# Optimization experiments

Hardware: AMD Instinct MI355X
Metric: run time of the kernel (lower is better)

Reference implementation:

```python
import jax, jax.numpy as jnp
import numpy as np

C = 128
K = 7
RED = 4
C_RED = C // RED
PAD = (K - 1) // 2
BN_EPS = 1e-5


def setup_inputs() -> dict:
    key = jax.random.key(0)
    ks = jax.random.split(key, 7)
    b, h, w = 8, 56, 56
    x = jax.random.normal(ks[0], (b, C, h, w), dtype=jnp.float32)
    # 1x1 conv #1: c -> c_red
    w1 = jax.random.normal(ks[1], (C_RED, C), dtype=jnp.float32) * (1.0 / np.sqrt(C))
    b1 = jax.random.normal(ks[2], (C_RED,), dtype=jnp.float32) * 0.01
    # BatchNorm affine params
    gamma = jnp.ones((C_RED,), dtype=jnp.float32)
    beta = jnp.zeros((C_RED,), dtype=jnp.float32)
    # 1x1 conv #2: c_red -> k*k
    w2 = jax.random.normal(ks[3], (K * K, C_RED), dtype=jnp.float32) * (1.0 / np.sqrt(C_RED))
    b2 = jax.random.normal(ks[4], (K * K,), dtype=jnp.float32) * 0.01
    return {"x": x, "w1": w1, "b1": b1, "gamma": gamma, "beta": beta, "w2": w2, "b2": b2}


def _unfold(x):
    # torch.nn.Unfold(K, padding=PAD, stride=1) -> (b, c, k*k, h, w), channel-major
    b, c, h, w = x.shape
    xp = jnp.pad(x, ((0, 0), (0, 0), (PAD, PAD), (PAD, PAD)))
    patches = [xp[:, :, i:i + h, j:j + w] for i in range(K) for j in range(K)]
    return jnp.stack(patches, axis=2)  # (b, c, k*k, h, w)


def reference(x, w1, b1, gamma, beta, w2, b2):
    b, c, h, w = x.shape
    # kernel-generation branch: 1x1 conv -> BN (batch stats, training mode) -> ReLU -> 1x1 conv
    t = jnp.einsum('rc,bchw->brhw', w1, x) + b1[None, :, None, None]
    mean = t.mean(axis=(0, 2, 3))
    var = t.var(axis=(0, 2, 3))  # biased, as in torch BN normalization
    t = (t - mean[None, :, None, None]) * jax.lax.rsqrt(var + BN_EPS)[None, :, None, None]
    t = jax.nn.relu(t * gamma[None, :, None, None] + beta[None, :, None, None])
    kern = jnp.einsum('kr,brhw->bkhw', w2, t) + b2[None, :, None, None]  # (b, k*k, h, w)
    # involution: per-pixel kernel broadcast over channels, sum over k*k taps
    x_unf = _unfold(x)  # (b, c, k*k, h, w)
    return jnp.einsum('bkhw,bckhw->bchw', kern, x_unf)
```

## Files before the change

### kernel.cpp

```cpp
#include <hip/hip_runtime.h>

#define C 128
#define CRED 32
#define K 7
#define KK 49
#define H 56
#define W 56
#define P (H*W)
#define B 8
#define NPIX (B*P)
#define BN_EPS 1e-5

#define T_OFF 0
#define T_SIZE (B*CRED*P)
#define KERN_OFF (T_OFF + T_SIZE)
#define KERN_SIZE (B*KK*P)
#define NBLK_A (49*B)
#define PSUM_OFF (KERN_OFF + KERN_SIZE)
#define PSQ_OFF (PSUM_OFF + NBLK_A*CRED)
#define SS_OFF  (PSQ_OFF + NBLK_A*CRED)
#define SCALE_OFF SS_OFF
#define SHIFT_OFF (SS_OFF + CRED)
#define WS_NEED ((size_t)(SHIFT_OFF + CRED) * sizeof(float))

#define FB_SCALE_OFF T_SIZE
#define FB_SHIFT_OFF (T_SIZE + CRED)

__global__ __launch_bounds__(256) void kA_conv1(const float* __restrict__ x,
                                                const float* __restrict__ w1,
                                                const float* __restrict__ b1,
                                                float* __restrict__ ws) {
    int tid = threadIdx.x;
    int bx = blockIdx.x;
    int b  = blockIdx.y;
    int px = tid & 63;
    int p  = bx * 64 + px;
    int ru8 = __builtin_amdgcn_readfirstlane((tid >> 6) * 8);
    const float* __restrict__ wq = w1 + (size_t)ru8 * C;
    const float* xb = x + (size_t)b * C * P + p;

    float acc[8];
#pragma unroll
    for (int u = 0; u < 8; ++u) acc[u] = 0.f;
#pragma unroll 8
    for (int c = 0; c < C; ++c) {
        float xv = xb[(size_t)c * P];
#pragma unroll
        for (int u = 0; u < 8; ++u)
            acc[u] = fmaf(wq[u * C + c], xv, acc[u]);
    }
#pragma unroll
    for (int u = 0; u < 8; ++u) acc[u] += b1[ru8 + u];

    float* tb = ws + T_OFF + (size_t)b * CRED * P + p;
#pragma unroll
    for (int u = 0; u < 8; ++u)
        tb[(size_t)(ru8 + u) * P] = acc[u];

    float s[8], q[8];
#pragma unroll
    for (int u = 0; u < 8; ++u) { s[u] = acc[u]; q[u] = acc[u] * acc[u]; }
#pragma unroll
    for (int off = 32; off; off >>= 1) {
#pragma unroll
        for (int u = 0; u < 8; ++u) {
            s[u] += __shfl_xor(s[u], off);
            q[u] += __shfl_xor(q[u], off);
        }
    }
    if (px == 0) {
        int blk = b * 49 + bx;
        float* psum = ws + PSUM_OFF + (size_t)blk * CRED + ru8;
        float* psq  = ws + PSQ_OFF  + (size_t)blk * CRED + ru8;
#pragma unroll
        for (int u = 0; u < 8; ++u) { psum[u] = s[u]; psq[u] = q[u]; }
    }
}

__global__ __launch_bounds__(256) void kB_bnfin(const float* __restrict__ gamma,
                                                const float* __restrict__ beta,
                                                float* __restrict__ ws) {
    __shared__ double sd1[8][CRED];
    __shared__ double sd2[8][CRED];
    int tid = threadIdx.x;
    int r = tid & 31, g = tid >> 5;
    double s1 = 0.0, s2 = 0.0;
    for (int i = g * 49; i < g * 49 + 49; ++i) {
        s1 += (double)ws[PSUM_OFF + i * CRED + r];
        s2 += (double)ws[PSQ_OFF + i * CRED + r];
    }
    sd1[g][r] = s1; sd2[g][r] = s2;
    __syncthreads();
    if (tid < CRED) {
        double S1 = 0.0, S2 = 0.0;
        for (int gg = 0; gg < 8; ++gg) { S1 += sd1[gg][tid]; S2 += sd2[gg][tid]; }
        double mean = S1 / NPIX;
        double var = S2 / NPIX - mean * mean;
        double sc = (double)gamma[tid] / sqrt(var + BN_EPS);
        ws[SCALE_OFF + tid] = (float)sc;
        ws[SHIFT_OFF + tid] = (float)((double)beta[tid] - mean * sc);
    }
}

__global__ __launch_bounds__(256) void kC_kern(const float* __restrict__ w2,
                                               const float* __restrict__ b2,
                                               float* __restrict__ ws) {
    __shared__ float s_t[CRED * W];
    __shared__ float s_w2[KK * 33];
    int tid = threadIdx.x;
    int h = blockIdx.x, b = blockIdx.y;
    for (int i = tid; i < KK * CRED; i += 256) {
        int k = i >> 5, r = i & 31;
        s_w2[k * 33 + r] = w2[i];
    }
    const float* scale = ws + SCALE_OFF;
    const float* shift = ws + SHIFT_OFF;
    for (int i = tid; i < CRED * W; i += 256) {
        int r = i / W, w = i - r * W;
        float v = ws[T_OFF + ((size_t)b * CRED + r) * P + h * W + w];
        v = fmaf(v, scale[r], shift[r]);
        s_t[r * W + w] = fmaxf(v, 0.f);
    }
    __syncthreads();
    for (int i = tid; i < KK * 14; i += 256) {
        int k = i / 14, w0 = (i - k * 14) * 4;
        float bb = b2[k];
        float a0 = bb, a1 = bb, a2 = bb, a3 = bb;
#pragma unroll
        for (int r = 0; r < CRED; ++r) {
            float4 tv = *(const float4*)&s_t[r * W + w0];
            float wv = s_w2[k * 33 + r];
            a0 = fmaf(wv, tv.x, a0);
            a1 = fmaf(wv, tv.y, a1);
            a2 = fmaf(wv, tv.z, a2);
            a3 = fmaf(wv, tv.w, a3);
        }
        float4 o = {a0, a1, a2, a3};
        *(float4*)&ws[KERN_OFF + ((size_t)b * KK + k) * P + h * W + w0] = o;
    }
}

#define TH 8
#define XROWS 14
#define XPITCH 68
__global__ __launch_bounds__(448) void kD_inv(const float* __restrict__ x,
                                              const float* __restrict__ ws,
                                              float* __restrict__ out) {
    __shared__ float4 s_x[2][XROWS * XPITCH];
    int tid = threadIdx.x;
    int bx = blockIdx.x;
    int z  = blockIdx.y;
    int b = bx / 7, ht = bx - b * 7;
    int h0 = ht * TH;
    int orow = tid / W;
    int ocol = tid - orow * W;
    int sbase = orow * XPITCH + ocol;

    float kr[KK];
    {
        const float* kb = ws + KERN_OFF + (size_t)b * KK * P + (size_t)h0 * W + tid;
#pragma unroll
        for (int k = 0; k < KK; ++k) kr[k] = kb[(size_t)k * P];
    }

    int slot0, slot1, off0, off1, v0, v1;
    {
        int q = tid;
        int row = q >> 6, col = q & 63;
        int hh = h0 - 3 + row, ww = col - 3;
        v0 = ((unsigned)hh < H && (unsigned)ww < W);
        off0 = hh * W + ww;
        slot0 = row * XPITCH + col;
        q = tid + 448;
        row = q >> 6; col = q & 63;
        hh = h0 - 3 + row; ww = col - 3;
        v1 = ((unsigned)hh < H && (unsigned)ww < W);
        off1 = hh * W + ww;
        slot1 = row * XPITCH + col;
    }

    int cg0 = z * 16;
    const size_t xbase = ((size_t)b * C + cg0) * P;
    {
        const float* xc = x + xbase;
        float4 f0, f1;
        f0.x = v0 ? xc[off0] : 0.f;  f0.y = v0 ? xc[P + off0] : 0.f;
        f0.z = v0 ? xc[2 * P + off0] : 0.f;  f0.w = v0 ? xc[3 * P + off0] : 0.f;
        f1.x = v1 ? xc[off1] : 0.f;  f1.y = v1 ? xc[P + off1] : 0.f;
        f1.z = v1 ? xc[2 * P + off1] : 0.f;  f1.w = v1 ? xc[3 * P + off1] : 0.f;
        s_x[0][slot0] = f0;
        s_x[0][slot1] = f1;
    }

    for (int it = 0; it < 4; ++it) {
        __syncthreads();
        float4 n0, n1;
        if (it < 3) {
            const float* xc = x + xbase + (size_t)(it + 1) * 4 * P;
            n0.x = v0 ? xc[off0] : 0.f;  n0.y = v0 ? xc[P + off0] : 0.f;
            n0.z = v0 ? xc[2 * P + off0] : 0.f;  n0.w = v0 ? xc[3 * P + off0] : 0.f;
            n1.x = v1 ? xc[off1] : 0.f;  n1.y = v1 ? xc[P + off1] : 0.f;
            n1.z = v1 ? xc[2 * P + off1] : 0.f;  n1.w = v1 ? xc[3 * P + off1] : 0.f;
        }
        const float4* xs = s_x[it & 1] + sbase;
        float a0 = 0.f, a1 = 0.f, a2 = 0.f, a3 = 0.f;
#pragma unroll
        for (int i = 0; i < K; ++i) {
#pragma unroll
            for (int j = 0; j < K; ++j) {
                float4 xv = xs[i * XPITCH + j];
                float kv = kr[i * 7 + j];
                a0 = fmaf(kv, xv.x, a0);
                a1 = fmaf(kv, xv.y, a1);
                a2 = fmaf(kv, xv.z, a2);
                a3 = fmaf(kv, xv.w, a3);
            }
        }
        float* ob = out + xbase + (size_t)it * 4 * P + (size_t)h0 * W + tid;
        ob[0]     = a0;
        ob[P]     = a1;
        ob[2 * P] = a2;
        ob[3 * P] = a3;
        if (it < 3) {
            float4* nb = s_x[(it + 1) & 1];
            nb[slot0] = n0;
            nb[slot1] = n1;
        }
    }
}

__global__ __launch_bounds__(256) void k1_conv1(const float* __restrict__ x,
                                                const float* __restrict__ w1,
                                                const float* __restrict__ b1,
                                                float* __restrict__ t) {
    __shared__ float s_w1t[C * CRED];
    int tid = threadIdx.x;
    for (int i = tid; i < C * CRED; i += 256) {
        int c = i >> 5, r = i & 31;
        s_w1t[i] = w1[r * C + c];
    }
    __syncthreads();
    int b = blockIdx.y;
    int p = blockIdx.x * 256 + tid;
    if (p >= P) return;
    float acc[CRED];
#pragma unroll
    for (int r = 0; r < CRED; ++r) acc[r] = 0.f;
    const float* xb = x + (size_t)b * C * P + p;
    for (int c = 0; c < C; ++c) {
        float xv = xb[(size_t)c * P];
#pragma unroll
        for (int r = 0; r < CRED; ++r)
            acc[r] = fmaf(s_w1t[c * CRED + r], xv, acc[r]);
    }
    float* tb = t + (size_t)b * CRED * P + p;
#pragma unroll
    for (int r = 0; r < CRED; ++r)
        tb[(size_t)r * P] = acc[r] + b1[r];
}

__global__ __launch_bounds__(256) void k2_bnstats(const float* __restrict__ t,
                                                  const float* __restrict__ gamma,
                                                  const float* __restrict__ beta,
                                                  float* __restrict__ scale,
                                                  float* __restrict__ shift) {
    int r = blockIdx.x;
    int tid = threadIdx.x;
    double s = 0.0, s2 = 0.0;
    for (int i = tid; i < NPIX; i += 256) {
        int b = i / P, p = i - b * P;
        float v = t[((size_t)b * CRED + r) * P + p];
        s += v;
        s2 += (double)v * v;
    }
    __shared__ double ls[256], ls2[256];
    ls[tid] = s; ls2[tid] = s2;
    __syncthreads();
    for (int off = 128; off > 0; off >>= 1) {
        if (tid < off) { ls[tid] += ls[tid + off]; ls2[tid] += ls2[tid + off]; }
        __syncthreads();
    }
    if (tid == 0) {
        double mean = ls[0] / NPIX;
        double var = ls2[0] / NPIX - mean * mean;
        double sc = (double)gamma[r] / sqrt(var + BN_EPS);
        scale[r] = (float)sc;
        shift[r] = (float)((double)beta[r] - mean * sc);
    }
}

__global__ __launch_bounds__(256) void k3_involution(const float* __restrict__ x,
                                                     const float* __restrict__ t,
                                                     const float* __restrict__ scale,
                                                     const float* __restrict__ shift,
                                                     const float* __restrict__ w2,
                                                     const float* __restrict__ b2,
                                                     float* __restrict__ out) {
    int h = blockIdx.x;
    int b = blockIdx.y;
    int z = blockIdx.z;
    int tid = threadIdx.x;
    __shared__ float s_w2[KK * CRED];
    __shared__ float s_t[CRED * W];
    __shared__ float s_kern[KK][W];
    __shared__ float s_x[4][K][64];
    for (int i = tid; i < KK * CRED; i += 256) s_w2[i] = w2[i];
    for (int i = tid; i < CRED * W; i += 256) {
        int r = i / W, w = i - r * W;
        float v = t[((size_t)b * CRED + r) * P + h * W + w];
        v = fmaf(v, scale[r], shift[r]);
        s_t[r * W + w] = fmaxf(v, 0.f);
    }
    __syncthreads();
    for (int i = tid; i < KK * W; i += 256) {
        int k = i / W, w = i - k * W;
        float acc = b2[k];
#pragma unroll
        for (int r = 0; r < CRED; ++r)
            acc = fmaf(s_w2[k * CRED + r], s_t[r * W + w], acc);
        s_kern[k][w] = acc;
    }
    __syncthreads();
    int w = tid % W;
    int c4 = tid / W;
    float kr[KK];
#pragma unroll
    for (int k = 0; k < KK; ++k) kr[k] = s_kern[k][w];
    int cbase = z * (C / 2);
    for (int cg = cbase; cg < cbase + C / 2; cg += 4) {
        for (int i = tid; i < 4 * K * 64; i += 256) {
            int col = i & 63;
            int rc = i >> 6;
            int cc = rc / K;
            int row = rc - cc * K;
            int hh = h - 3 + row;
            int ww = col - 3;
            float v = 0.f;
            if ((unsigned)hh < H && (unsigned)ww < W)
                v = x[(((size_t)b * C + cg + cc) * H + hh) * W + ww];
            s_x[cc][row][col] = v;
        }
        __syncthreads();
        if (tid < 4 * W) {
            float acc = 0.f;
#pragma unroll
            for (int i = 0; i < K; ++i)
#pragma unroll
                for (int j = 0; j < K; ++j)
                    acc = fmaf(kr[i * K + j], s_x[c4][i][w + j], acc);
            out[(((size_t)b * C + cg + c4) * H + h) * W + w] = acc;
        }
        __syncthreads();
    }
}

extern "C" void kernel_launch(void* const* d_in, const int* in_sizes, int n_in,
                              void* d_out, int out_size, void* d_ws, size_t ws_size,
                              hipStream_t stream) {
    const float* x     = (const float*)d_in[0];
    const float* w1    = (const float*)d_in[1];
    const float* b1    = (const float*)d_in[2];
    const float* gamma = (const float*)d_in[3];
    const float* beta  = (const float*)d_in[4];
    const float* w2    = (const float*)d_in[5];
    const float* b2    = (const float*)d_in[6];
    float* out = (float*)d_out;
    float* ws  = (float*)d_ws;

    if (ws_size >= WS_NEED) {
        dim3 gA(49, B);
        kA_conv1<<<gA, 256, 0, stream>>>(x, w1, b1, ws);
        kB_bnfin<<<1, 256, 0, stream>>>(gamma, beta, ws);
        dim3 gC(H, B);
        kC_kern<<<gC, 256, 0, stream>>>(w2, b2, ws);
        dim3 gD(7 * B, 8);
        kD_inv<<<gD, 448, 0, stream>>>(x, ws, out);
    } else {
        float* t     = ws;
        float* scale = ws + FB_SCALE_OFF;
        float* shift = ws + FB_SHIFT_OFF;
        dim3 g1((P + 255) / 256, B);
        k1_conv1<<<g1, 256, 0, stream>>>(x, w1, b1, t);
        k2_bnstats<<<CRED, 256, 0, stream>>>(t, gamma, beta, scale, shift);
        dim3 g3(H, B, 2);
        k3_involution<<<g3, 256, 0, stream>>>(x, t, scale, shift, w2, b2, out);
    }
}
```

Before: 44.42 us.

## Fuse BN finalize into kernel-gen kernel and retile involution to 7-row tiles

Removes the single-block BN finalize launch: every kernel-generation block now redundantly reduces the per-block partial sums to get scale and shift in shared memory, while loading the raw t tile in parallel. The involution kernel changes from 8-row to 7-row tiles (64 blocks per channel group), so 392 of 448 threads compute and the rest only help load the halo. Masked loads are replaced by clamped-offset loads multiplied by a 0/1 mask. This saves one launch and its serialization, at the cost of 448 blocks each repeating the 392x32 partial reduction in double precision and more involution blocks with idle threads.

```diff
diff --git a/kernel.cpp b/kernel.cpp
--- a/kernel.cpp
+++ b/kernel.cpp
@@ -77,49 +77,51 @@
     }
 }
 
-__global__ __launch_bounds__(256) void kB_bnfin(const float* __restrict__ gamma,
+__global__ __launch_bounds__(256) void kCB_kern(const float* __restrict__ w2,
+                                                const float* __restrict__ b2,
+                                                const float* __restrict__ gamma,
                                                 const float* __restrict__ beta,
                                                 float* __restrict__ ws) {
+    __shared__ float s_t[CRED * W];
+    __shared__ float s_w2[KK * 33];
     __shared__ double sd1[8][CRED];
     __shared__ double sd2[8][CRED];
-    int tid = threadIdx.x;
-    int r = tid & 31, g = tid >> 5;
-    double s1 = 0.0, s2 = 0.0;
-    for (int i = g * 49; i < g * 49 + 49; ++i) {
-        s1 += (double)ws[PSUM_OFF + i * CRED + r];
-        s2 += (double)ws[PSQ_OFF + i * CRED + r];
-    }
-    sd1[g][r] = s1; sd2[g][r] = s2;
+    __shared__ float s_sc[CRED];
+    __shared__ float s_sh[CRED];
+    int tid = threadIdx.x;
+    int h = blockIdx.x, b = blockIdx.y;
+
+    {
+        int r = tid & 31, seg = tid >> 5;
+        double s1 = 0.0, s2 = 0.0;
+        for (int i = seg * 49; i < seg * 49 + 49; ++i) {
+            s1 += (double)ws[PSUM_OFF + i * CRED + r];
+            s2 += (double)ws[PSQ_OFF + i * CRED + r];
+        }
+        sd1[seg][r] = s1; sd2[seg][r] = s2;
+    }
+    for (int i = tid; i < KK * CRED; i += 256) {
+        int k = i >> 5, r = i & 31;
+        s_w2[k * 33 + r] = w2[i];
+    }
+    for (int i = tid; i < CRED * W; i += 256) {
+        int r = i / W, w = i - r * W;
+        s_t[i] = ws[T_OFF + ((size_t)b * CRED + r) * P + h * W + w];
+    }
     __syncthreads();
     if (tid < CRED) {
         double S1 = 0.0, S2 = 0.0;
-        for (int gg = 0; gg < 8; ++gg) { S1 += sd1[gg][tid]; S2 += sd2[gg][tid]; }
+        for (int g = 0; g < 8; ++g) { S1 += sd1[g][tid]; S2 += sd2[g][tid]; }
         double mean = S1 / NPIX;
         double var = S2 / NPIX - mean * mean;
         double sc = (double)gamma[tid] / sqrt(var + BN_EPS);
-        ws[SCALE_OFF + tid] = (float)sc;
-        ws[SHIFT_OFF + tid] = (float)((double)beta[tid] - mean * sc);
-    }
-}
-
-__global__ __launch_bounds__(256) void kC_kern(const float* __restrict__ w2,
-                                               const float* __restrict__ b2,
-                                               float* __restrict__ ws) {
-    __shared__ float s_t[CRED * W];
-    __shared__ float s_w2[KK * 33];
-    int tid = threadIdx.x;
-    int h = blockIdx.x, b = blockIdx.y;
-    for (int i = tid; i < KK * CRED; i += 256) {
-        int k = i >> 5, r = i & 31;
-        s_w2[k * 33 + r] = w2[i];
-    }
-    const float* scale = ws + SCALE_OFF;
-    const float* shift = ws + SHIFT_OFF;
+        s_sc[tid] = (float)sc;
+        s_sh[tid] = (float)((double)beta[tid] - mean * sc);
+    }
+    __syncthreads();
     for (int i = tid; i < CRED * W; i += 256) {
-        int r = i / W, w = i - r * W;
-        float v = ws[T_OFF + ((size_t)b * CRED + r) * P + h * W + w];
-        v = fmaf(v, scale[r], shift[r]);
-        s_t[r * W + w] = fmaxf(v, 0.f);
+        int r = i / W;
+        s_t[i] = fmaxf(fmaf(s_t[i], s_sc[r], s_sh[r]), 0.f);
     }
     __syncthreads();
     for (int i = tid; i < KK * 14; i += 256) {
@@ -140,8 +142,8 @@
     }
 }
 
-#define TH 8
-#define XROWS 14
+#define TH 7
+#define XROWS 13
 #define XPITCH 68
 __global__ __launch_bounds__(448) void kD_inv(const float* __restrict__ x,
                                               const float* __restrict__ ws,
@@ -150,81 +152,83 @@
     int tid = threadIdx.x;
     int bx = blockIdx.x;
     int z  = blockIdx.y;
-    int b = bx / 7, ht = bx - b * 7;
+    int b = bx >> 3, ht = bx & 7;
     int h0 = ht * TH;
     int orow = tid / W;
     int ocol = tid - orow * W;
     int sbase = orow * XPITCH + ocol;
+    bool owns = orow < TH;
+
+    int q0 = tid, q1 = tid + 448;
+    int row0 = q0 >> 6, col0 = q0 & 63;
+    int hh0 = h0 - 3 + row0, ww0 = col0 - 3;
+    float m0 = ((unsigned)hh0 < H && (unsigned)ww0 < W) ? 1.f : 0.f;
+    int off0 = (m0 != 0.f) ? (hh0 * W + ww0) : 0;
+    int slot0 = row0 * XPITCH + col0;
+    int row1 = q1 >> 6, col1 = q1 & 63;
+    int hh1 = h0 - 3 + row1, ww1 = col1 - 3;
+    bool in1 = q1 < XROWS * 64;
+    float m1 = (in1 && (unsigned)hh1 < H && (unsigned)ww1 < W) ? 1.f : 0.f;
+    int off1 = (m1 != 0.f) ? (hh1 * W + ww1) : 0;
+    int slot1 = row1 * XPITCH + col1;
+
+    int cg0 = z * 16;
+    const size_t xbase = ((size_t)b * C + cg0) * P;
+
+    const float* xc0 = x + xbase;
+    float4 f0, f1;
+    f0.x = xc0[off0] * m0;          f0.y = xc0[P + off0] * m0;
+    f0.z = xc0[2 * P + off0] * m0;  f0.w = xc0[3 * P + off0] * m0;
+    f1.x = xc0[off1] * m1;          f1.y = xc0[P + off1] * m1;
+    f1.z = xc0[2 * P + off1] * m1;  f1.w = xc0[3 * P + off1] * m1;
 
     float kr[KK];
     {
-        const float* kb = ws + KERN_OFF + (size_t)b * KK * P + (size_t)h0 * W + tid;
+        int kidx = h0 * W + tid;
+        if (kidx > P - 1) kidx = P - 1;
+        const float* kb = ws + KERN_OFF + (size_t)b * KK * P + kidx;
 #pragma unroll
         for (int k = 0; k < KK; ++k) kr[k] = kb[(size_t)k * P];
     }
 
-    int slot0, slot1, off0, off1, v0, v1;
-    {
-        int q = tid;
-        int row = q >> 6, col = q & 63;
-        int hh = h0 - 3 + row, ww = col - 3;
-        v0 = ((unsigned)hh < H && (unsigned)ww < W);
-        off0 = hh * W + ww;
-        slot0 = row * XPITCH + col;
-        q = tid + 448;
-        row = q >> 6; col = q & 63;
-        hh = h0 - 3 + row; ww = col - 3;
-        v1 = ((unsigned)hh < H && (unsigned)ww < W);
-        off1 = hh * W + ww;
-        slot1 = row * XPITCH + col;
-    }
-
-    int cg0 = z * 16;
-    const size_t xbase = ((size_t)b * C + cg0) * P;
-    {
-        const float* xc = x + xbase;
-        float4 f0, f1;
-        f0.x = v0 ? xc[off0] : 0.f;  f0.y = v0 ? xc[P + off0] : 0.f;
-        f0.z = v0 ? xc[2 * P + off0] : 0.f;  f0.w = v0 ? xc[3 * P + off0] : 0.f;
-        f1.x = v1 ? xc[off1] : 0.f;  f1.y = v1 ? xc[P + off1] : 0.f;
-        f1.z = v1 ? xc[2 * P + off1] : 0.f;  f1.w = v1 ? xc[3 * P + off1] : 0.f;
-        s_x[0][slot0] = f0;
-        s_x[0][slot1] = f1;
-    }
+    s_x[0][slot0] = f0;
+    if (in1) s_x[0][slot1] = f1;
 
     for (int it = 0; it < 4; ++it) {
         __syncthreads();
         float4 n0, n1;
         if (it < 3) {
             const float* xc = x + xbase + (size_t)(it + 1) * 4 * P;
-            n0.x = v0 ? xc[off0] : 0.f;  n0.y = v0 ? xc[P + off0] : 0.f;
-            n0.z = v0 ? xc[2 * P + off0] : 0.f;  n0.w = v0 ? xc[3 * P + off0] : 0.f;
-            n1.x = v1 ? xc[off1] : 0.f;  n1.y = v1 ? xc[P + off1] : 0.f;
-            n1.z = v1 ? xc[2 * P + off1] : 0.f;  n1.w = v1 ? xc[3 * P + off1] : 0.f;
-        }
-        const float4* xs = s_x[it & 1] + sbase;
-        float a0 = 0.f, a1 = 0.f, a2 = 0.f, a3 = 0.f;
-#pragma unroll
-        for (int i = 0; i < K; ++i) {
-#pragma unroll
-            for (int j = 0; j < K; ++j) {
-                float4 xv = xs[i * XPITCH + j];
-                float kv = kr[i * 7 + j];
-                a0 = fmaf(kv, xv.x, a0);
-                a1 = fmaf(kv, xv.y, a1);
-                a2 = fmaf(kv, xv.z, a2);
-                a3 = fmaf(kv, xv.w, a3);
+            n0.x = xc[off0] * m0;          n0.y = xc[P + off0] * m0;
+            n0.z = xc[2 * P + off0] * m0;  n0.w = xc[3 * P + off0] * m0;
+            n1.x = xc[off1] * m1;          n1.y = xc[P + off1] * m1;
+            n1.z = xc[2 * P + off1] * m1;  n1.w = xc[3 * P + off1] * m1;
+        }
+        if (owns) {
+            const float4* xs = s_x[it & 1] + sbase;
+            float a0 = 0.f, a1 = 0.f, a2 = 0.f, a3 = 0.f;
+#pragma unroll
+            for (int i = 0; i < K; ++i) {
+#pragma unroll
+                for (int j = 0; j < K; ++j) {
+                    float4 xv = xs[i * XPITCH + j];
+                    float kv = kr[i * 7 + j];
+                    a0 = fmaf(kv, xv.x, a0);
+                    a1 = fmaf(kv, xv.y, a1);
+                    a2 = fmaf(kv, xv.z, a2);
+                    a3 = fmaf(kv, xv.w, a3);
+                }
             }
-        }
-        float* ob = out + xbase + (size_t)it * 4 * P + (size_t)h0 * W + tid;
-        ob[0]     = a0;
-        ob[P]     = a1;
-        ob[2 * P] = a2;
-        ob[3 * P] = a3;
+            float* ob = out + xbase + (size_t)it * 4 * P + (size_t)h0 * W + tid;
+            ob[0]     = a0;
+            ob[P]     = a1;
+            ob[2 * P] = a2;
+            ob[3 * P] = a3;
+        }
         if (it < 3) {
             float4* nb = s_x[(it + 1) & 1];
             nb[slot0] = n0;
-            nb[slot1] = n1;
+            if (in1) nb[slot1] = n1;
         }
     }
 }
@@ -370,10 +374,9 @@
     if (ws_size >= WS_NEED) {
         dim3 gA(49, B);
         kA_conv1<<<gA, 256, 0, stream>>>(x, w1, b1, ws);
-        kB_bnfin<<<1, 256, 0, stream>>>(gamma, beta, ws);
         dim3 gC(H, B);
-        kC_kern<<<gC, 256, 0, stream>>>(w2, b2, ws);
-        dim3 gD(7 * B, 8);
+        kCB_kern<<<gC, 256, 0, stream>>>(w2, b2, gamma, beta, ws);
+        dim3 gD(64, 8);
         kD_inv<<<gD, 448, 0, stream>>>(x, ws, out);
     } else {
         float* t     = ws;
```

New measurement: 48.46 us. 9.1% more time.

## Process 32 channels per block with single-shot LDS load in involution kernel

Applied to the files above, without the earlier changes.

The involution kernel now stages all 32 channels of a block's input tile into shared memory at once, instead of double-buffering 4 channels at a time over 16 channels. Each thread keeps 8 float4 accumulators and streams the per-pixel kernel weights from global memory per tap, so each weight read is reused across 32 channels. The grid is halved along the channel dimension. This removes the per-iteration barriers and reuses each weight more, but needs about 119 KB of LDS per block, which limits occupancy to one block per CU. The smaller grid also no longer covers all CUs, and the staging load no longer overlaps with compute.

```diff
diff --git a/kernel.cpp b/kernel.cpp
--- a/kernel.cpp
+++ b/kernel.cpp
@@ -143,10 +143,10 @@
 #define TH 8
 #define XROWS 14
 #define XPITCH 68
-__global__ __launch_bounds__(448) void kD_inv(const float* __restrict__ x,
-                                              const float* __restrict__ ws,
-                                              float* __restrict__ out) {
-    __shared__ float4 s_x[2][XROWS * XPITCH];
+__global__ __launch_bounds__(448) void kD2_inv(const float* __restrict__ x,
+                                               const float* __restrict__ ws,
+                                               float* __restrict__ out) {
+    __shared__ float4 s_x[XROWS * 8 * XPITCH];
     int tid = threadIdx.x;
     int bx = blockIdx.x;
     int z  = blockIdx.y;
@@ -154,78 +154,64 @@
     int h0 = ht * TH;
     int orow = tid / W;
     int ocol = tid - orow * W;
-    int sbase = orow * XPITCH + ocol;
-
-    float kr[KK];
-    {
-        const float* kb = ws + KERN_OFF + (size_t)b * KK * P + (size_t)h0 * W + tid;
-#pragma unroll
-        for (int k = 0; k < KK; ++k) kr[k] = kb[(size_t)k * P];
-    }
-
-    int slot0, slot1, off0, off1, v0, v1;
-    {
-        int q = tid;
-        int row = q >> 6, col = q & 63;
-        int hh = h0 - 3 + row, ww = col - 3;
-        v0 = ((unsigned)hh < H && (unsigned)ww < W);
-        off0 = hh * W + ww;
-        slot0 = row * XPITCH + col;
-        q = tid + 448;
-        row = q >> 6; col = q & 63;
-        hh = h0 - 3 + row; ww = col - 3;
-        v1 = ((unsigned)hh < H && (unsigned)ww < W);
-        off1 = hh * W + ww;
-        slot1 = row * XPITCH + col;
-    }
-
-    int cg0 = z * 16;
+
+    int row0 = tid >> 6, col0 = tid & 63;
+    int hh0 = h0 - 3 + row0, ww0 = col0 - 3;
+    float m0 = ((unsigned)hh0 < H && (unsigned)ww0 < W) ? 1.f : 0.f;
+    int off0 = (m0 != 0.f) ? (hh0 * W + ww0) : 0;
+    int hh1 = hh0 + 7;
+    float m1 = ((unsigned)hh1 < H && (unsigned)ww0 < W) ? 1.f : 0.f;
+    int off1 = (m1 != 0.f) ? (hh1 * W + ww0) : 0;
+    int slot0b = (row0 * 8) * XPITCH + col0;
+    int slot1b = ((row0 + 7) * 8) * XPITCH + col0;
+
+    int cg0 = z * 32;
     const size_t xbase = ((size_t)b * C + cg0) * P;
-    {
-        const float* xc = x + xbase;
+
+#pragma unroll
+    for (int g = 0; g < 8; ++g) {
+        const float* xc = x + xbase + (size_t)(4 * g) * P;
         float4 f0, f1;
-        f0.x = v0 ? xc[off0] : 0.f;  f0.y = v0 ? xc[P + off0] : 0.f;
-        f0.z = v0 ? xc[2 * P + off0] : 0.f;  f0.w = v0 ? xc[3 * P + off0] : 0.f;
-        f1.x = v1 ? xc[off1] : 0.f;  f1.y = v1 ? xc[P + off1] : 0.f;
-        f1.z = v1 ? xc[2 * P + off1] : 0.f;  f1.w = v1 ? xc[3 * P + off1] : 0.f;
-        s_x[0][slot0] = f0;
-        s_x[0][slot1] = f1;
-    }
-
-    for (int it = 0; it < 4; ++it) {
-        __syncthreads();
-        float4 n0, n1;
-        if (it < 3) {
-            const float* xc = x + xbase + (size_t)(it + 1) * 4 * P;
-            n0.x = v0 ? xc[off0] : 0.f;  n0.y = v0 ? xc[P + off0] : 0.f;
-            n0.z = v0 ? xc[2 * P + off0] : 0.f;  n0.w = v0 ? xc[3 * P + off0] : 0.f;
-            n1.x = v1 ? xc[off1] : 0.f;  n1.y = v1 ? xc[P + off1] : 0.f;
-            n1.z = v1 ? xc[2 * P + off1] : 0.f;  n1.w = v1 ? xc[3 * P + off1] : 0.f;
-        }
-        const float4* xs = s_x[it & 1] + sbase;
-        float a0 = 0.f, a1 = 0.f, a2 = 0.f, a3 = 0.f;
-#pragma unroll
-        for (int i = 0; i < K; ++i) {
-#pragma unroll
-            for (int j = 0; j < K; ++j) {
-                float4 xv = xs[i * XPITCH + j];
-                float kv = kr[i * 7 + j];
-                a0 = fmaf(kv, xv.x, a0);
-                a1 = fmaf(kv, xv.y, a1);
-                a2 = fmaf(kv, xv.z, a2);
-                a3 = fmaf(kv, xv.w, a3);
+        f0.x = xc[off0] * m0;          f0.y = xc[P + off0] * m0;
+        f0.z = xc[2 * P + off0] * m0;  f0.w = xc[3 * P + off0] * m0;
+        f1.x = xc[off1] * m1;          f1.y = xc[P + off1] * m1;
+        f1.z = xc[2 * P + off1] * m1;  f1.w = xc[3 * P + off1] * m1;
+        s_x[slot0b + g * XPITCH] = f0;
+        s_x[slot1b + g * XPITCH] = f1;
+    }
+    __syncthreads();
+
+    int p0 = h0 * W + tid;
+    const float* kp = ws + KERN_OFF + (size_t)b * KK * P + p0;
+
+    float4 acc[8];
+#pragma unroll
+    for (int g = 0; g < 8; ++g) acc[g] = make_float4(0.f, 0.f, 0.f, 0.f);
+
+    const float4* xs = s_x + orow * (8 * XPITCH) + ocol;
+    for (int i = 0; i < K; ++i) {
+        const float4* xr = xs + i * (8 * XPITCH);
+#pragma unroll
+        for (int j = 0; j < K; ++j) {
+            float kv = kp[(size_t)(i * 7 + j) * P];
+#pragma unroll
+            for (int g = 0; g < 8; ++g) {
+                float4 xv = xr[g * XPITCH + j];
+                acc[g].x = fmaf(kv, xv.x, acc[g].x);
+                acc[g].y = fmaf(kv, xv.y, acc[g].y);
+                acc[g].z = fmaf(kv, xv.z, acc[g].z);
+                acc[g].w = fmaf(kv, xv.w, acc[g].w);
             }
         }
-        float* ob = out + xbase + (size_t)it * 4 * P + (size_t)h0 * W + tid;
-        ob[0]     = a0;
-        ob[P]     = a1;
-        ob[2 * P] = a2;
-        ob[3 * P] = a3;
-        if (it < 3) {
-            float4* nb = s_x[(it + 1) & 1];
-            nb[slot0] = n0;
-            nb[slot1] = n1;
-        }
+    }
+
+#pragma unroll
+    for (int g = 0; g < 8; ++g) {
+        float* ob = out + xbase + (size_t)(4 * g) * P + p0;
+        ob[0]     = acc[g].x;
+        ob[P]     = acc[g].y;
+        ob[2 * P] = acc[g].z;
+        ob[3 * P] = acc[g].w;
     }
 }
 
@@ -373,8 +359,8 @@
         kB_bnfin<<<1, 256, 0, stream>>>(gamma, beta, ws);
         dim3 gC(H, B);
         kC_kern<<<gC, 256, 0, stream>>>(w2, b2, ws);
-        dim3 gD(7 * B, 8);
-        kD_inv<<<gD, 448, 0, stream>>>(x, ws, out);
+        dim3 gD(7 * B, 4);
+        kD2_inv<<<gD, 448, 0, stream>>>(x, ws, out);
     } else {
         float* t     = ws;
         float* scale = ws + FB_SCALE_OFF;
```

Result: slower. 48.85 us (+10.0%).
